# Kernel optimization log

Measured on AMD Instinct MI355X. Metric: run time of the kernel, lower is better.

The kernel has to match this reference:

```python
import jax, jax.numpy as jnp
import numpy as np

L, H, Wn, C = 2048, 768, 1024, 64


def setup_inputs() -> dict:
    key = jax.random.key(0)
    ks = jax.random.split(key, 12)
    s = 1.0 / np.sqrt(H)
    s3 = 1.0 / np.sqrt(3 * H)
    return {
        "tok_embs": jax.random.normal(ks[0], (L, H), jnp.float32),
        "wmask": jax.random.randint(ks[1], (L,), 0, Wn + 1),  # 1-indexed word positions, 0 = ignore
        "text_length": Wn,
        "label_embs": jax.random.normal(ks[2], (C, H), jnp.float32),
        "W_tok": jax.random.normal(ks[3], (H, 2 * H), jnp.float32) * s,
        "b_tok": jnp.zeros((2 * H,), jnp.float32),
        "W_lab": jax.random.normal(ks[4], (H, 2 * H), jnp.float32) * s,
        "b_lab": jnp.zeros((2 * H,), jnp.float32),
        "W1": jax.random.normal(ks[5], (3 * H, H), jnp.float32) * s3,
        "b1": jnp.zeros((H,), jnp.float32),
        "W2": jax.random.normal(ks[6], (H, 3), jnp.float32) * s,
        "b2": jnp.zeros((3,), jnp.float32),
    }


def reference(tok_embs, wmask, text_length, label_embs, W_tok, b_tok, W_lab, b_lab, W1, b1, W2, b2):
    Wd = text_length
    Hd = tok_embs.shape[-1]
    # --- word-level scatter pooling: we[wmask-1] = tok_embs where wmask > 0 ---
    # route masked-out tokens to a dummy row Wd, then drop it (jit-safe, no nonzero)
    tgt = jnp.where(wmask > 0, wmask - 1, Wd)
    we = jnp.zeros((Wd + 1, Hd), tok_embs.dtype).at[tgt].set(tok_embs)[:Wd]  # (W, H)
    # --- scorer ---
    t = (we @ W_tok + b_tok).reshape(Wd, 2, Hd)        # (W, 2, H)
    lb = (label_embs @ W_lab + b_lab).reshape(-1, 2, Hd)  # (C, 2, H)
    Cd = lb.shape[0]
    t0 = jnp.broadcast_to(t[:, None, 0, :], (Wd, Cd, Hd))
    l0 = jnp.broadcast_to(lb[None, :, 0, :], (Wd, Cd, Hd))
    prod = t[:, None, 1, :] * lb[None, :, 1, :]        # (W, C, H)
    cat = jnp.concatenate([t0, l0, prod], axis=-1)     # (W, C, 3H)
    h = jax.nn.relu(cat @ W1 + b1)                     # (W, C, H)
    scores = h @ W2 + b2                               # (W, C, 3)
    return scores
```

## Files before the change

### kernel.cpp

```cpp
#include <hip/hip_runtime.h>
#include <hip/hip_bf16.h>

static constexpr int Hd = 768;
static constexpr int H2 = 1536;
static constexpr int Cn = 64;

typedef __attribute__((ext_vector_type(8))) short short8;
typedef __attribute__((ext_vector_type(8))) _Float16 half8;
typedef __attribute__((ext_vector_type(4))) float f32x4;
typedef unsigned short us;

__device__ inline unsigned int f2bf2(float a, float b) {
    __hip_bfloat162 h = __float22bfloat162_rn(float2{a, b});
    return *reinterpret_cast<unsigned int*>(&h);
}

__device__ inline void split1(float x, us& h, us& l) {
    __hip_bfloat16 hb = __float2bfloat16(x);
    float hf = __bfloat162float(hb);
    __hip_bfloat16 lb_ = __float2bfloat16(x - hf);
    h = *reinterpret_cast<us*>(&hb);
    l = *reinterpret_cast<us*>(&lb_);
}

__device__ inline us f2b(float x) {
    __hip_bfloat16 b = __float2bfloat16(x);
    return *reinterpret_cast<us*>(&b);
}

__device__ inline us f2h(float x) {
    _Float16 h = (_Float16)x;
    return *reinterpret_cast<us*>(&h);
}

__device__ inline float b2f(us u) {
    __hip_bfloat16 b = *reinterpret_cast<__hip_bfloat16*>(&u);
    return __bfloat162float(b);
}

__device__ inline short8 hmul8(short8 a, short8 b) {
    half8 x = __builtin_bit_cast(half8, a);
    half8 y = __builtin_bit_cast(half8, b);
    half8 r = x * y;
    return __builtin_bit_cast(short8, r);
}

__device__ inline int swz(int row, int q) {
    return row * 32 + ((q ^ ((row >> 1) & 3)) << 3);
}

__device__ inline void gload16(const void* g, void* l) {
    __builtin_amdgcn_global_load_lds(
        (const __attribute__((address_space(1))) unsigned int*)g,
        (__attribute__((address_space(3))) unsigned int*)l, 16, 0, 0);
}

__global__ void k_init(int* widx, int Wd) {
    int i = blockIdx.x * 256 + threadIdx.x;
    if (i < Wd) widx[i] = -1;
}

__global__ void k_scatter(const int* __restrict__ wmask, int* widx, int L, int Wd) {
    int i = blockIdx.x * 256 + threadIdx.x;
    if (i < L) {
        int m = wmask[i];
        if (m > 0 && m <= Wd) atomicMax(&widx[m - 1], i);
    }
}

__global__ void k_build_we_split(const float4* __restrict__ tok, const int* __restrict__ widx,
                                 us* __restrict__ weh, us* __restrict__ wel, int Wd) {
    int i = blockIdx.x * 256 + threadIdx.x;
    if (i >= Wd * 192) return;
    int w = i / 192, c4 = i - w * 192;
    int idx = widx[w];
    float4 v = (idx >= 0) ? tok[idx * 192 + c4] : float4{0.f, 0.f, 0.f, 0.f};
    us hh[4], ll[4];
    split1(v.x, hh[0], ll[0]);
    split1(v.y, hh[1], ll[1]);
    split1(v.z, hh[2], ll[2]);
    split1(v.w, hh[3], ll[3]);
    size_t o = (size_t)w * Hd + c4 * 4;
    *(ushort4*)&weh[o] = ushort4{hh[0], hh[1], hh[2], hh[3]};
    *(ushort4*)&wel[o] = ushort4{ll[0], ll[1], ll[2], ll[3]};
}

struct TSArgs {
    const float* src[5];
    us* th[5];
    us* tl[5];
    int ld[5];
    int N[5];
    int fmt[5];
};
__global__ __launch_bounds__(256)
void k_tsplit(TSArgs a) {
    __shared__ float tile[64][65];
    const int z = blockIdx.z;
    const int n0 = blockIdx.x * 64, k0 = blockIdx.y * 64;
    if (n0 >= a.N[z]) return;
    const float* W = a.src[z];
    const int ld = a.ld[z];
    for (int idx = threadIdx.x; idx < 4096; idx += 256) {
        int kk = idx >> 6, nn = idx & 63;
        tile[kk][nn] = W[(size_t)(k0 + kk) * ld + n0 + nn];
    }
    __syncthreads();
    us* Th = a.th[z];
    us* Tl = a.tl[z];
    const int fmt = a.fmt[z];
    for (int idx = threadIdx.x; idx < 4096; idx += 256) {
        int nn = idx >> 6, kk = idx & 63;
        size_t o = (size_t)(n0 + nn) * Hd + k0 + kk;
        if (fmt) {
            Th[o] = f2h(tile[kk][nn]);
        } else {
            us h, l;
            split1(tile[kk][nn], h, l);
            Th[o] = h;
            Tl[o] = l;
        }
    }
}

__global__ __launch_bounds__(256)
void k_split(const float* __restrict__ x, int lda, int cols,
             us* __restrict__ h, us* __restrict__ l, int n4) {
    int i = blockIdx.x * 256 + threadIdx.x;
    if (i >= n4) return;
    int c4 = cols >> 2;
    int row = i / c4, cc = (i - row * c4) * 4;
    float4 v = *(const float4*)&x[(size_t)row * lda + cc];
    us hh[4], ll[4];
    split1(v.x, hh[0], ll[0]);
    split1(v.y, hh[1], ll[1]);
    split1(v.z, hh[2], ll[2]);
    split1(v.w, hh[3], ll[3]);
    size_t o = (size_t)row * cols + cc;
    *(ushort4*)&h[o] = ushort4{hh[0], hh[1], hh[2], hh[3]};
    *(ushort4*)&l[o] = ushort4{ll[0], ll[1], ll[2], ll[3]};
}

__global__ __launch_bounds__(256)
void k_gemm2(const us* __restrict__ Ah, const us* __restrict__ Al,
             const us* __restrict__ BhT, const us* __restrict__ BlT,
             float* __restrict__ Cpart, int M, int N, int K) {
    __shared__ __align__(16) us S[2][4][64 * 32];
    const int tid = threadIdx.x, wave = tid >> 6, lane = tid & 63;
    const int quad = lane >> 4, l15 = lane & 15;
    const int wm = wave & 1, wn = wave >> 1;
    const int m0 = blockIdx.y * 64, n0 = blockIdx.x * 64;
    const int Ks = K / gridDim.z, kbeg = blockIdx.z * Ks, kend = kbeg + Ks;
    float* C = Cpart + (size_t)blockIdx.z * M * N;

    const int srow = wave * 16 + (lane >> 2), soff = (lane & 3) * 8;
    const size_t gaB = (size_t)(m0 + srow) * K + soff;
    const size_t gbB = (size_t)(n0 + srow) * K + soff;
    const int lo = wave * 16 * 32;

    f32x4 acc[2][2];
#pragma unroll
    for (int a = 0; a < 2; ++a)
#pragma unroll
        for (int b = 0; b < 2; ++b) acc[a][b] = (f32x4){0.f, 0.f, 0.f, 0.f};

    auto stage = [&](int p, int k0) {
        gload16(Ah + gaB + k0, &S[p][0][lo]);
        gload16(Al + gaB + k0, &S[p][1][lo]);
        gload16(BhT + gbB + k0, &S[p][2][lo]);
        gload16(BlT + gbB + k0, &S[p][3][lo]);
    };

    int p = 0;
    stage(0, kbeg);
    for (int k0 = kbeg; k0 < kend; k0 += 32) {
        __syncthreads();
        if (k0 + 32 < kend) stage(p ^ 1, k0 + 32);
        short8 ah[2], al[2], bh[2], bl[2];
#pragma unroll
        for (int mt = 0; mt < 2; ++mt) {
            int off = (wm * 32 + mt * 16 + l15) * 32 + quad * 8;
            ah[mt] = *(const short8*)&S[p][0][off];
            al[mt] = *(const short8*)&S[p][1][off];
        }
#pragma unroll
        for (int nt = 0; nt < 2; ++nt) {
            int off = (wn * 32 + nt * 16 + l15) * 32 + quad * 8;
            bh[nt] = *(const short8*)&S[p][2][off];
            bl[nt] = *(const short8*)&S[p][3][off];
        }
#pragma unroll
        for (int mt = 0; mt < 2; ++mt)
#pragma unroll
            for (int nt = 0; nt < 2; ++nt) {
                acc[mt][nt] = __builtin_amdgcn_mfma_f32_16x16x32_bf16(al[mt], bh[nt], acc[mt][nt], 0, 0, 0);
                acc[mt][nt] = __builtin_amdgcn_mfma_f32_16x16x32_bf16(ah[mt], bl[nt], acc[mt][nt], 0, 0, 0);
                acc[mt][nt] = __builtin_amdgcn_mfma_f32_16x16x32_bf16(ah[mt], bh[nt], acc[mt][nt], 0, 0, 0);
            }
        p ^= 1;
    }
#pragma unroll
    for (int mt = 0; mt < 2; ++mt)
#pragma unroll
        for (int nt = 0; nt < 2; ++nt) {
            int col = n0 + wn * 32 + nt * 16 + l15;
#pragma unroll
            for (int reg = 0; reg < 4; ++reg) {
                int row = m0 + wm * 32 + mt * 16 + quad * 4 + reg;
                C[(size_t)row * N + col] = acc[mt][nt][reg];
            }
        }
}

__global__ __launch_bounds__(256)
void k_gemm3(const us* __restrict__ Ah, const us* __restrict__ Al,
             const us* __restrict__ BhT, const us* __restrict__ BlT,
             const float* __restrict__ bias, float* __restrict__ outF,
             us* __restrict__ sh, us* __restrict__ sl, us* __restrict__ bh16,
             int fp16out, int scols, int N, int K) {
    __shared__ __align__(16) us S[2][4][64 * 32];
    const int tid = threadIdx.x, wave = tid >> 6, lane = tid & 63;
    const int quad = lane >> 4, l15 = lane & 15;
    const int wm = wave & 1, wn = wave >> 1;
    const int m0 = blockIdx.y * 64, n0 = blockIdx.x * 64;

    const int srow = wave * 16 + (lane >> 2), soff = (lane & 3) * 8;
    const size_t gaB = (size_t)(m0 + srow) * K + soff;
    const size_t gbB = (size_t)(n0 + srow) * K + soff;
    const int lo = wave * 16 * 32;

    f32x4 acc[2][2];
#pragma unroll
    for (int a = 0; a < 2; ++a)
#pragma unroll
        for (int b = 0; b < 2; ++b) acc[a][b] = (f32x4){0.f, 0.f, 0.f, 0.f};

    auto stage = [&](int p, int k0) {
        gload16(Ah + gaB + k0, &S[p][0][lo]);
        gload16(Al + gaB + k0, &S[p][1][lo]);
        gload16(BhT + gbB + k0, &S[p][2][lo]);
        gload16(BlT + gbB + k0, &S[p][3][lo]);
    };

    int p = 0;
    stage(0, 0);
    for (int k0 = 0; k0 < K; k0 += 32) {
        __syncthreads();
        if (k0 + 32 < K) stage(p ^ 1, k0 + 32);
        short8 ah[2], al[2], bh[2], bl[2];
#pragma unroll
        for (int mt = 0; mt < 2; ++mt) {
            int off = (wm * 32 + mt * 16 + l15) * 32 + quad * 8;
            ah[mt] = *(const short8*)&S[p][0][off];
            al[mt] = *(const short8*)&S[p][1][off];
        }
#pragma unroll
        for (int nt = 0; nt < 2; ++nt) {
            int off = (wn * 32 + nt * 16 + l15) * 32 + quad * 8;
            bh[nt] = *(const short8*)&S[p][2][off];
            bl[nt] = *(const short8*)&S[p][3][off];
        }
#pragma unroll
        for (int mt = 0; mt < 2; ++mt)
#pragma unroll
            for (int nt = 0; nt < 2; ++nt) {
                acc[mt][nt] = __builtin_amdgcn_mfma_f32_16x16x32_bf16(al[mt], bh[nt], acc[mt][nt], 0, 0, 0);
                acc[mt][nt] = __builtin_amdgcn_mfma_f32_16x16x32_bf16(ah[mt], bl[nt], acc[mt][nt], 0, 0, 0);
                acc[mt][nt] = __builtin_amdgcn_mfma_f32_16x16x32_bf16(ah[mt], bh[nt], acc[mt][nt], 0, 0, 0);
            }
        p ^= 1;
    }
#pragma unroll
    for (int mt = 0; mt < 2; ++mt)
#pragma unroll
        for (int nt = 0; nt < 2; ++nt) {
            int col = n0 + wn * 32 + nt * 16 + l15;
            float bb = bias ? bias[col] : 0.f;
#pragma unroll
            for (int reg = 0; reg < 4; ++reg) {
                int row = m0 + wm * 32 + mt * 16 + quad * 4 + reg;
                float v = acc[mt][nt][reg] + bb;
                if (outF) outF[(size_t)row * N + col] = v;
                if (sh) {
                    if (col < scols) {
                        us h, l;
                        split1(v, h, l);
                        size_t o = (size_t)row * scols + col;
                        sh[o] = h;
                        sl[o] = l;
                    } else if (bh16) {
                        bh16[(size_t)row * scols + (col - scols)] = fp16out ? f2h(v) : f2b(v);
                    }
                }
            }
        }
}

__global__ __launch_bounds__(256)
void k_reduce(const float* __restrict__ part, int S, int MN, int N,
              const float* __restrict__ bias, float* __restrict__ outF,
              us* __restrict__ sh, us* __restrict__ sl, int scols,
              us* __restrict__ bh16, int fp16out) {
    int i = blockIdx.x * 256 + threadIdx.x;
    if (i >= MN) return;
    float v = 0.f;
    for (int s = 0; s < S; ++s) v += part[(size_t)s * MN + i];
    int row = i / N, col = i - row * N;
    if (bias) v += bias[col];
    if (outF) outF[i] = v;
    if (col < scols) {
        if (sh) {
            us h, l;
            split1(v, h, l);
            size_t o = (size_t)row * scols + col;
            sh[o] = h;
            sl[o] = l;
        }
    } else if (bh16) {
        bh16[(size_t)row * scols + (col - scols)] = fp16out ? f2h(v) : f2b(v);
    }
}

__global__ __launch_bounds__(256, 3)
void k_mfma7(const us* __restrict__ t1b,
             const us* __restrict__ W1ct,
             const us* __restrict__ lb1b,
             const float* __restrict__ Aw,
             const float* __restrict__ Bc,
             const float* __restrict__ W2,
             float* __restrict__ scr) {
    __shared__ __align__(16) us As[2][128 * 32];
    __shared__ __align__(16) us Bs[2][128 * 32];
    __shared__ float sred[128 * 3];

    const int tid = threadIdx.x, wave = tid >> 6, lane = tid & 63;
    const int quad = lane >> 4, l15 = lane & 15;
    const int wm = wave & 1, wn = wave >> 1;

    const int b = blockIdx.x;
    const int xcd = b & 7, slot = b >> 3;
    const int jx = slot >> 6;
    const int c = slot & 63;
    const int my = xcd;
    const int jt = jx * 128, m0 = my * 128;

    for (int i = tid; i < 128 * 3; i += 256) sred[i] = 0.f;

    const int aro = tid >> 1;
    const int qb = (tid & 1) * 2;
    const int kbase = qb * 8;
    const us* gA = W1ct + (size_t)(jt + aro) * Hd + kbase;
    const us* gL = lb1b + (size_t)c * Hd + kbase;
    const us* gB = t1b + (size_t)(m0 + aro) * Hd + kbase;
    const int w0 = swz(aro, qb), w1 = swz(aro, qb + 1);

    f32x4 acc[4][4];
#pragma unroll
    for (int mt = 0; mt < 4; ++mt)
#pragma unroll
        for (int nt = 0; nt < 4; ++nt) acc[mt][nt] = (f32x4){0.f, 0.f, 0.f, 0.f};

    short8 aw0l, aw0h, al0l, al0h, b0l, b0h;
    short8 aw1l, aw1h, al1l, al1h, b1l, b1h;

    aw0l = *(const short8*)(gA + 0);  aw0h = *(const short8*)(gA + 8);
    al0l = *(const short8*)(gL + 0);  al0h = *(const short8*)(gL + 8);
    b0l  = *(const short8*)(gB + 0);  b0h  = *(const short8*)(gB + 8);
    aw1l = *(const short8*)(gA + 32); aw1h = *(const short8*)(gA + 40);
    al1l = *(const short8*)(gL + 32); al1h = *(const short8*)(gL + 40);
    b1l  = *(const short8*)(gB + 32); b1h  = *(const short8*)(gB + 40);
    *(short8*)&As[0][w0] = hmul8(aw0l, al0l);
    *(short8*)&As[0][w1] = hmul8(aw0h, al0h);
    *(short8*)&Bs[0][w0] = b0l;
    *(short8*)&Bs[0][w1] = b0h;
    __syncthreads();

    for (int k = 0; k < Hd; k += 64) {
        {
            short8 af[4], bf[4];
#pragma unroll
            for (int mt = 0; mt < 4; ++mt)
                af[mt] = *(const short8*)&As[0][swz(wm * 64 + mt * 16 + l15, quad)];
#pragma unroll
            for (int nt = 0; nt < 4; ++nt)
                bf[nt] = *(const short8*)&Bs[0][swz(wn * 64 + nt * 16 + l15, quad)];
            if (k + 64 < Hd) {
                aw0l = *(const short8*)(gA + k + 64); aw0h = *(const short8*)(gA + k + 72);
                al0l = *(const short8*)(gL + k + 64); al0h = *(const short8*)(gL + k + 72);
                b0l  = *(const short8*)(gB + k + 64); b0h  = *(const short8*)(gB + k + 72);
            }
#pragma unroll
            for (int mt = 0; mt < 4; ++mt)
#pragma unroll
                for (int nt = 0; nt < 4; ++nt)
                    acc[mt][nt] = __builtin_amdgcn_mfma_f32_16x16x32_f16(
                        __builtin_bit_cast(half8, af[mt]),
                        __builtin_bit_cast(half8, bf[nt]), acc[mt][nt], 0, 0, 0);
            *(short8*)&As[1][w0] = hmul8(aw1l, al1l);
            *(short8*)&As[1][w1] = hmul8(aw1h, al1h);
            *(short8*)&Bs[1][w0] = b1l;
            *(short8*)&Bs[1][w1] = b1h;
            __syncthreads();
        }
        {
            short8 af[4], bf[4];
#pragma unroll
            for (int mt = 0; mt < 4; ++mt)
                af[mt] = *(const short8*)&As[1][swz(wm * 64 + mt * 16 + l15, quad)];
#pragma unroll
            for (int nt = 0; nt < 4; ++nt)
                bf[nt] = *(const short8*)&Bs[1][swz(wn * 64 + nt * 16 + l15, quad)];
            if (k + 96 < Hd) {
                aw1l = *(const short8*)(gA + k + 96); aw1h = *(const short8*)(gA + k + 104);
                al1l = *(const short8*)(gL + k + 96); al1h = *(const short8*)(gL + k + 104);
                b1l  = *(const short8*)(gB + k + 96); b1h  = *(const short8*)(gB + k + 104);
            }
#pragma unroll
            for (int mt = 0; mt < 4; ++mt)
#pragma unroll
                for (int nt = 0; nt < 4; ++nt)
                    acc[mt][nt] = __builtin_amdgcn_mfma_f32_16x16x32_f16(
                        __builtin_bit_cast(half8, af[mt]),
                        __builtin_bit_cast(half8, bf[nt]), acc[mt][nt], 0, 0, 0);
            if (k + 64 < Hd) {
                *(short8*)&As[0][w0] = hmul8(aw0l, al0l);
                *(short8*)&As[0][w1] = hmul8(aw0h, al0h);
                *(short8*)&Bs[0][w0] = b0l;
                *(short8*)&Bs[0][w1] = b0h;
                __syncthreads();
            }
        }
    }

    float bcv[4][4], w2v[4][4][3];
#pragma unroll
    for (int mt = 0; mt < 4; ++mt) {
        const int jb = jt + wm * 64 + mt * 16 + quad * 4;
        float4 b4 = *(const float4*)&Bc[(size_t)c * Hd + jb];
        bcv[mt][0] = b4.x; bcv[mt][1] = b4.y; bcv[mt][2] = b4.z; bcv[mt][3] = b4.w;
#pragma unroll
        for (int reg = 0; reg < 4; ++reg)
#pragma unroll
            for (int r = 0; r < 3; ++r) w2v[mt][reg][r] = W2[(jb + reg) * 3 + r];
    }
#pragma unroll
    for (int nt = 0; nt < 4; ++nt) {
        const int w = m0 + wn * 64 + nt * 16 + l15;
        const float* awp = Aw + (size_t)w * Hd + jt + wm * 64;
        float s0 = 0.f, s1 = 0.f, s2 = 0.f;
#pragma unroll
        for (int mt = 0; mt < 4; ++mt) {
            float4 a4 = *(const float4*)&awp[mt * 16 + quad * 4];
            float av[4] = {a4.x, a4.y, a4.z, a4.w};
#pragma unroll
            for (int reg = 0; reg < 4; ++reg) {
                float h = acc[mt][nt][reg] + av[reg] + bcv[mt][reg];
                h = h > 0.f ? h : 0.f;
                s0 += h * w2v[mt][reg][0];
                s1 += h * w2v[mt][reg][1];
                s2 += h * w2v[mt][reg][2];
            }
        }
        s0 += __shfl_xor(s0, 16); s0 += __shfl_xor(s0, 32);
        s1 += __shfl_xor(s1, 16); s1 += __shfl_xor(s1, 32);
        s2 += __shfl_xor(s2, 16); s2 += __shfl_xor(s2, 32);
        if (quad == 0) {
            const int wl = wn * 64 + nt * 16 + l15;
            atomicAdd(&sred[wl * 3 + 0], s0);
            atomicAdd(&sred[wl * 3 + 1], s1);
            atomicAdd(&sred[wl * 3 + 2], s2);
        }
    }
    __syncthreads();
    float* slab = scr + ((size_t)jx * 1024 * Cn + (size_t)m0 * Cn + c) * 3;
    for (int i = tid; i < 128 * 3; i += 256) {
        int wl = i / 3, r = i - wl * 3;
        slab[(size_t)wl * Cn * 3 + r] = sred[i];
    }
}

__global__ __launch_bounds__(256)
void k_scores(const float* __restrict__ scr, const float* __restrict__ b2,
              float* __restrict__ out, int n) {
    int i = blockIdx.x * 256 + threadIdx.x;
    if (i >= n) return;
    float v = b2[i % 3];
#pragma unroll
    for (int s = 0; s < 6; ++s) v += scr[(size_t)s * n + i];
    out[i] = v;
}

extern "C" void kernel_launch(void* const* d_in, const int* in_sizes, int n_in,
                              void* d_out, int out_size, void* d_ws, size_t ws_size,
                              hipStream_t stream) {
    const float* tok    = (const float*)d_in[0];
    const int*   wmask  = (const int*)d_in[1];
    const float* labe   = (const float*)d_in[3];
    const float* W_tok  = (const float*)d_in[4];
    const float* b_tok  = (const float*)d_in[5];
    const float* W_lab  = (const float*)d_in[6];
    const float* b_lab  = (const float*)d_in[7];
    const float* W1     = (const float*)d_in[8];
    const float* b1     = (const float*)d_in[9];
    const float* W2     = (const float*)d_in[10];
    const float* b2     = (const float*)d_in[11];
    float* out = (float*)d_out;

    const int L  = in_sizes[1];
    const int Wd = out_size / (Cn * 3);

    char* ws = (char*)d_ws;
    size_t off = 0;
    auto alloc = [&](size_t bytes) { char* p = ws + off; off += (bytes + 255) & ~(size_t)255; return p; };
    int*   widx  = (int*)alloc(4096);
    float* Abuf  = (float*)alloc((size_t)Wd * Hd * 4);
    float* Bbuf  = (float*)alloc((size_t)Cn * Hd * 4);
    us* W1ct  = (us*)alloc((size_t)Hd * Hd * 2);
    us* W1cl  = (us*)alloc((size_t)Hd * Hd * 2);
    us* t1b   = (us*)alloc((size_t)Wd * Hd * 2);
    us* lb1b  = (us*)alloc((size_t)Cn * Hd * 2);
    float* scr = (float*)alloc((size_t)6 * Wd * Cn * 3 * 4);
    us* WtTh  = (us*)alloc((size_t)H2 * Hd * 2);
    us* WtTl  = (us*)alloc((size_t)H2 * Hd * 2);
    us* WlTh  = (us*)alloc((size_t)H2 * Hd * 2);
    us* WlTl  = (us*)alloc((size_t)H2 * Hd * 2);
    us* W1aTh = (us*)alloc((size_t)Hd * Hd * 2);
    us* W1aTl = (us*)alloc((size_t)Hd * Hd * 2);
    us* W1bTh = (us*)alloc((size_t)Hd * Hd * 2);
    us* W1bTl = (us*)alloc((size_t)Hd * Hd * 2);
    us* weh   = (us*)alloc((size_t)Wd * Hd * 2);
    us* wel   = (us*)alloc((size_t)Wd * Hd * 2);
    us* lah   = (us*)alloc((size_t)Cn * Hd * 2);
    us* lal   = (us*)alloc((size_t)Cn * Hd * 2);
    us* t0h   = (us*)alloc((size_t)Wd * Hd * 2);
    us* t0l   = (us*)alloc((size_t)Wd * Hd * 2);
    us* lb0h  = (us*)alloc((size_t)Cn * Hd * 2);
    us* lb0l  = (us*)alloc((size_t)Cn * Hd * 2);
    float* part = (float*)alloc((size_t)8 * Cn * H2 * 4);

    k_init<<<(Wd + 255) / 256, 256, 0, stream>>>(widx, Wd);
    k_scatter<<<(L + 255) / 256, 256, 0, stream>>>(wmask, widx, L, Wd);
    k_build_we_split<<<(Wd * 192 + 255) / 256, 256, 0, stream>>>((const float4*)tok, widx, weh, wel, Wd);

    TSArgs ts;
    ts.src[0] = W_tok;  ts.th[0] = WtTh;  ts.tl[0] = WtTl;  ts.ld[0] = H2; ts.N[0] = H2; ts.fmt[0] = 0;
    ts.src[1] = W_lab;  ts.th[1] = WlTh;  ts.tl[1] = WlTl;  ts.ld[1] = H2; ts.N[1] = H2; ts.fmt[1] = 0;
    ts.src[2] = W1;                         ts.th[2] = W1aTh; ts.tl[2] = W1aTl; ts.ld[2] = Hd; ts.N[2] = Hd; ts.fmt[2] = 0;
    ts.src[3] = W1 + (size_t)Hd * Hd;       ts.th[3] = W1bTh; ts.tl[3] = W1bTl; ts.ld[3] = Hd; ts.N[3] = Hd; ts.fmt[3] = 0;
    ts.src[4] = W1 + (size_t)2 * Hd * Hd;   ts.th[4] = W1ct;  ts.tl[4] = W1cl;  ts.ld[4] = Hd; ts.N[4] = Hd; ts.fmt[4] = 1;
    k_tsplit<<<dim3(H2 / 64, Hd / 64, 5), 256, 0, stream>>>(ts);

    k_split<<<(Cn * Hd / 4 + 255) / 256, 256, 0, stream>>>(labe, Hd, Hd, lah, lal, Cn * Hd / 4);

    k_gemm3<<<dim3(H2 / 64, Wd / 64), 256, 0, stream>>>(weh, wel, WtTh, WtTl, b_tok,
                                                        nullptr, t0h, t0l, t1b, 1, Hd, H2, Hd);

    k_gemm2<<<dim3(H2 / 64, 1, 8), 256, 0, stream>>>(lah, lal, WlTh, WlTl, part, Cn, H2, Hd);
    k_reduce<<<(Cn * H2 + 255) / 256, 256, 0, stream>>>(part, 8, Cn * H2, H2, b_lab, nullptr, lb0h, lb0l, Hd, lb1b, 1);

    k_gemm3<<<dim3(Hd / 64, Wd / 64), 256, 0, stream>>>(t0h, t0l, W1aTh, W1aTl, nullptr,
                                                        Abuf, nullptr, nullptr, nullptr, 0, 0, Hd, Hd);

    k_gemm2<<<dim3(Hd / 64, 1, 8), 256, 0, stream>>>(lb0h, lb0l, W1bTh, W1bTl, part, Cn, Hd, Hd);
    k_reduce<<<(Cn * Hd + 255) / 256, 256, 0, stream>>>(part, 8, Cn * Hd, Hd, b1, Bbuf, nullptr, nullptr, Hd, nullptr, 0);

    k_mfma7<<<3072, 256, 0, stream>>>(t1b, W1ct, lb1b, Abuf, Bbuf, W2, scr);

    k_scores<<<(Wd * Cn * 3 + 255) / 256, 256, 0, stream>>>(scr, b2, out, Wd * Cn * 3);
}
```

Before: 263.9 us.

## Process two labels per block with shared tiles and direct global-to-LDS loads

The main MFMA kernel now handles two labels per block, so each staged W1c and t1 tile feeds two accumulator sets. The label-weight elementwise product moves from staging into the inner loop, applied to register fragments from a small LDS copy of both label rows. Tiles are staged with async global_load_lds over a 32-wide K double buffer, replacing the register-staged swizzled layout. The aim is to halve global and LDS staging traffic per MFMA and cut grid size, at the cost of doubled accumulator registers, lower occupancy (2 blocks per CU) and extra half-precision multiplies in the hot loop.

```diff
diff --git a/kernel.cpp b/kernel.cpp
--- a/kernel.cpp
+++ b/kernel.cpp
@@ -43,10 +43,6 @@
     half8 y = __builtin_bit_cast(half8, b);
     half8 r = x * y;
     return __builtin_bit_cast(short8, r);
-}
-
-__device__ inline int swz(int row, int q) {
-    return row * 32 + ((q ^ ((row >> 1) & 3)) << 3);
 }
 
 __device__ inline void gload16(const void* g, void* l) {
@@ -321,17 +317,18 @@
     }
 }
 
-__global__ __launch_bounds__(256, 3)
-void k_mfma7(const us* __restrict__ t1b,
+__global__ __launch_bounds__(256, 2)
+void k_mfma8(const us* __restrict__ t1b,
              const us* __restrict__ W1ct,
              const us* __restrict__ lb1b,
              const float* __restrict__ Aw,
              const float* __restrict__ Bc,
              const float* __restrict__ W2,
              float* __restrict__ scr) {
-    __shared__ __align__(16) us As[2][128 * 32];
-    __shared__ __align__(16) us Bs[2][128 * 32];
-    __shared__ float sred[128 * 3];
+    __shared__ __align__(16) us As[2][4096];
+    __shared__ __align__(16) us Bs[2][4096];
+    __shared__ __align__(16) us lbs[2][Hd];
+    __shared__ float sred[2 * 128 * 3];
 
     const int tid = threadIdx.x, wave = tid >> 6, lane = tid & 63;
     const int quad = lane >> 4, l15 = lane & 15;
@@ -339,143 +336,123 @@
 
     const int b = blockIdx.x;
     const int xcd = b & 7, slot = b >> 3;
-    const int jx = slot >> 6;
-    const int c = slot & 63;
-    const int my = xcd;
-    const int jt = jx * 128, m0 = my * 128;
-
-    for (int i = tid; i < 128 * 3; i += 256) sred[i] = 0.f;
-
-    const int aro = tid >> 1;
-    const int qb = (tid & 1) * 2;
-    const int kbase = qb * 8;
-    const us* gA = W1ct + (size_t)(jt + aro) * Hd + kbase;
-    const us* gL = lb1b + (size_t)c * Hd + kbase;
-    const us* gB = t1b + (size_t)(m0 + aro) * Hd + kbase;
-    const int w0 = swz(aro, qb), w1 = swz(aro, qb + 1);
-
-    f32x4 acc[4][4];
+    const int jx = slot >> 5;
+    const int cp = slot & 31;
+    const int c0 = cp * 2;
+    const int jt = jx * 128, m0 = xcd * 128;
+
+    for (int i = tid; i < 2 * 128 * 3; i += 256) sred[i] = 0.f;
+    if (tid < 192) {
+        int cc = tid / 96, o = (tid - cc * 96) * 8;
+        *(short8*)&lbs[cc][o] = *(const short8*)&lb1b[(size_t)(c0 + cc) * Hd + o];
+    }
+
+    const int srow = (wave & 1) * 64 + lane;
+    const int skq = (wave >> 1) * 8;
+    const us* gA = W1ct + (size_t)(jt + srow) * Hd + skq;
+    const us* gB = t1b + (size_t)(m0 + srow) * Hd + skq;
+
+    f32x4 acc0[4][4], acc1[4][4];
 #pragma unroll
     for (int mt = 0; mt < 4; ++mt)
 #pragma unroll
-        for (int nt = 0; nt < 4; ++nt) acc[mt][nt] = (f32x4){0.f, 0.f, 0.f, 0.f};
-
-    short8 aw0l, aw0h, al0l, al0h, b0l, b0h;
-    short8 aw1l, aw1h, al1l, al1h, b1l, b1h;
-
-    aw0l = *(const short8*)(gA + 0);  aw0h = *(const short8*)(gA + 8);
-    al0l = *(const short8*)(gL + 0);  al0h = *(const short8*)(gL + 8);
-    b0l  = *(const short8*)(gB + 0);  b0h  = *(const short8*)(gB + 8);
-    aw1l = *(const short8*)(gA + 32); aw1h = *(const short8*)(gA + 40);
-    al1l = *(const short8*)(gL + 32); al1h = *(const short8*)(gL + 40);
-    b1l  = *(const short8*)(gB + 32); b1h  = *(const short8*)(gB + 40);
-    *(short8*)&As[0][w0] = hmul8(aw0l, al0l);
-    *(short8*)&As[0][w1] = hmul8(aw0h, al0h);
-    *(short8*)&Bs[0][w0] = b0l;
-    *(short8*)&Bs[0][w1] = b0h;
-    __syncthreads();
-
-    for (int k = 0; k < Hd; k += 64) {
-        {
-            short8 af[4], bf[4];
-#pragma unroll
-            for (int mt = 0; mt < 4; ++mt)
-                af[mt] = *(const short8*)&As[0][swz(wm * 64 + mt * 16 + l15, quad)];
-#pragma unroll
-            for (int nt = 0; nt < 4; ++nt)
-                bf[nt] = *(const short8*)&Bs[0][swz(wn * 64 + nt * 16 + l15, quad)];
-            if (k + 64 < Hd) {
-                aw0l = *(const short8*)(gA + k + 64); aw0h = *(const short8*)(gA + k + 72);
-                al0l = *(const short8*)(gL + k + 64); al0h = *(const short8*)(gL + k + 72);
-                b0l  = *(const short8*)(gB + k + 64); b0h  = *(const short8*)(gB + k + 72);
-            }
-#pragma unroll
-            for (int mt = 0; mt < 4; ++mt)
-#pragma unroll
-                for (int nt = 0; nt < 4; ++nt)
-                    acc[mt][nt] = __builtin_amdgcn_mfma_f32_16x16x32_f16(
-                        __builtin_bit_cast(half8, af[mt]),
-                        __builtin_bit_cast(half8, bf[nt]), acc[mt][nt], 0, 0, 0);
-            *(short8*)&As[1][w0] = hmul8(aw1l, al1l);
-            *(short8*)&As[1][w1] = hmul8(aw1h, al1h);
-            *(short8*)&Bs[1][w0] = b1l;
-            *(short8*)&Bs[1][w1] = b1h;
-            __syncthreads();
-        }
-        {
-            short8 af[4], bf[4];
-#pragma unroll
-            for (int mt = 0; mt < 4; ++mt)
-                af[mt] = *(const short8*)&As[1][swz(wm * 64 + mt * 16 + l15, quad)];
-#pragma unroll
-            for (int nt = 0; nt < 4; ++nt)
-                bf[nt] = *(const short8*)&Bs[1][swz(wn * 64 + nt * 16 + l15, quad)];
-            if (k + 96 < Hd) {
-                aw1l = *(const short8*)(gA + k + 96); aw1h = *(const short8*)(gA + k + 104);
-                al1l = *(const short8*)(gL + k + 96); al1h = *(const short8*)(gL + k + 104);
-                b1l  = *(const short8*)(gB + k + 96); b1h  = *(const short8*)(gB + k + 104);
-            }
-#pragma unroll
-            for (int mt = 0; mt < 4; ++mt)
-#pragma unroll
-                for (int nt = 0; nt < 4; ++nt)
-                    acc[mt][nt] = __builtin_amdgcn_mfma_f32_16x16x32_f16(
-                        __builtin_bit_cast(half8, af[mt]),
-                        __builtin_bit_cast(half8, bf[nt]), acc[mt][nt], 0, 0, 0);
-            if (k + 64 < Hd) {
-                *(short8*)&As[0][w0] = hmul8(aw0l, al0l);
-                *(short8*)&As[0][w1] = hmul8(aw0h, al0h);
-                *(short8*)&Bs[0][w0] = b0l;
-                *(short8*)&Bs[0][w1] = b0h;
-                __syncthreads();
-            }
-        }
-    }
-
-    float bcv[4][4], w2v[4][4][3];
+        for (int nt = 0; nt < 4; ++nt) {
+            acc0[mt][nt] = (f32x4){0.f, 0.f, 0.f, 0.f};
+            acc1[mt][nt] = (f32x4){0.f, 0.f, 0.f, 0.f};
+        }
+
+    auto stage = [&](int p, int k0) {
+        gload16(gA + k0,      &As[p][wave * 512]);
+        gload16(gA + k0 + 16, &As[p][(wave + 4) * 512]);
+        gload16(gB + k0,      &Bs[p][wave * 512]);
+        gload16(gB + k0 + 16, &Bs[p][(wave + 4) * 512]);
+    };
+
+    const int rbA = quad * 1024 + (wm * 64 + l15) * 8;
+    const int rbB = quad * 1024 + (wn * 64 + l15) * 8;
+
+    stage(0, 0);
+    int p = 0;
+    for (int k0 = 0; k0 < Hd; k0 += 32) {
+        __syncthreads();
+        if (k0 + 32 < Hd) stage(p ^ 1, k0 + 32);
+        short8 af[4], bf[4];
+#pragma unroll
+        for (int mt = 0; mt < 4; ++mt) af[mt] = *(const short8*)&As[p][rbA + mt * 128];
+#pragma unroll
+        for (int nt = 0; nt < 4; ++nt) bf[nt] = *(const short8*)&Bs[p][rbB + nt * 128];
+        short8 lv0 = *(const short8*)&lbs[0][k0 + quad * 8];
+        short8 lv1 = *(const short8*)&lbs[1][k0 + quad * 8];
+#pragma unroll
+        for (int mt = 0; mt < 4; ++mt) {
+            short8 a0 = hmul8(af[mt], lv0);
+            short8 a1 = hmul8(af[mt], lv1);
+#pragma unroll
+            for (int nt = 0; nt < 4; ++nt) {
+                acc0[mt][nt] = __builtin_amdgcn_mfma_f32_16x16x32_f16(
+                    __builtin_bit_cast(half8, a0),
+                    __builtin_bit_cast(half8, bf[nt]), acc0[mt][nt], 0, 0, 0);
+                acc1[mt][nt] = __builtin_amdgcn_mfma_f32_16x16x32_f16(
+                    __builtin_bit_cast(half8, a1),
+                    __builtin_bit_cast(half8, bf[nt]), acc1[mt][nt], 0, 0, 0);
+            }
+        }
+        p ^= 1;
+    }
+
+    float bcv0[4][4], bcv1[4][4], w2v[4][4][3];
 #pragma unroll
     for (int mt = 0; mt < 4; ++mt) {
         const int jb = jt + wm * 64 + mt * 16 + quad * 4;
-        float4 b4 = *(const float4*)&Bc[(size_t)c * Hd + jb];
-        bcv[mt][0] = b4.x; bcv[mt][1] = b4.y; bcv[mt][2] = b4.z; bcv[mt][3] = b4.w;
+        float4 b4 = *(const float4*)&Bc[(size_t)c0 * Hd + jb];
+        bcv0[mt][0] = b4.x; bcv0[mt][1] = b4.y; bcv0[mt][2] = b4.z; bcv0[mt][3] = b4.w;
+        float4 b5 = *(const float4*)&Bc[(size_t)(c0 + 1) * Hd + jb];
+        bcv1[mt][0] = b5.x; bcv1[mt][1] = b5.y; bcv1[mt][2] = b5.z; bcv1[mt][3] = b5.w;
 #pragma unroll
         for (int reg = 0; reg < 4; ++reg)
 #pragma unroll
             for (int r = 0; r < 3; ++r) w2v[mt][reg][r] = W2[(jb + reg) * 3 + r];
     }
-#pragma unroll
-    for (int nt = 0; nt < 4; ++nt) {
-        const int w = m0 + wn * 64 + nt * 16 + l15;
-        const float* awp = Aw + (size_t)w * Hd + jt + wm * 64;
-        float s0 = 0.f, s1 = 0.f, s2 = 0.f;
-#pragma unroll
-        for (int mt = 0; mt < 4; ++mt) {
-            float4 a4 = *(const float4*)&awp[mt * 16 + quad * 4];
-            float av[4] = {a4.x, a4.y, a4.z, a4.w};
-#pragma unroll
-            for (int reg = 0; reg < 4; ++reg) {
-                float h = acc[mt][nt][reg] + av[reg] + bcv[mt][reg];
-                h = h > 0.f ? h : 0.f;
-                s0 += h * w2v[mt][reg][0];
-                s1 += h * w2v[mt][reg][1];
-                s2 += h * w2v[mt][reg][2];
-            }
-        }
-        s0 += __shfl_xor(s0, 16); s0 += __shfl_xor(s0, 32);
-        s1 += __shfl_xor(s1, 16); s1 += __shfl_xor(s1, 32);
-        s2 += __shfl_xor(s2, 16); s2 += __shfl_xor(s2, 32);
-        if (quad == 0) {
-            const int wl = wn * 64 + nt * 16 + l15;
-            atomicAdd(&sred[wl * 3 + 0], s0);
-            atomicAdd(&sred[wl * 3 + 1], s1);
-            atomicAdd(&sred[wl * 3 + 2], s2);
-        }
-    }
+
+    auto reduce_c = [&](const f32x4 (&ac)[4][4], const float (&bcv)[4][4], int cc) {
+#pragma unroll
+        for (int nt = 0; nt < 4; ++nt) {
+            const int w = m0 + wn * 64 + nt * 16 + l15;
+            const float* awp = Aw + (size_t)w * Hd + jt + wm * 64;
+            float s0 = 0.f, s1 = 0.f, s2 = 0.f;
+#pragma unroll
+            for (int mt = 0; mt < 4; ++mt) {
+                float4 a4 = *(const float4*)&awp[mt * 16 + quad * 4];
+                float av[4] = {a4.x, a4.y, a4.z, a4.w};
+#pragma unroll
+                for (int reg = 0; reg < 4; ++reg) {
+                    float h = ac[mt][nt][reg] + av[reg] + bcv[mt][reg];
+                    h = h > 0.f ? h : 0.f;
+                    s0 += h * w2v[mt][reg][0];
+                    s1 += h * w2v[mt][reg][1];
+                    s2 += h * w2v[mt][reg][2];
+                }
+            }
+            s0 += __shfl_xor(s0, 16); s0 += __shfl_xor(s0, 32);
+            s1 += __shfl_xor(s1, 16); s1 += __shfl_xor(s1, 32);
+            s2 += __shfl_xor(s2, 16); s2 += __shfl_xor(s2, 32);
+            if (quad == 0) {
+                const int wl = wn * 64 + nt * 16 + l15;
+                atomicAdd(&sred[cc * 384 + wl * 3 + 0], s0);
+                atomicAdd(&sred[cc * 384 + wl * 3 + 1], s1);
+                atomicAdd(&sred[cc * 384 + wl * 3 + 2], s2);
+            }
+        }
+    };
+    reduce_c(acc0, bcv0, 0);
+    reduce_c(acc1, bcv1, 1);
     __syncthreads();
-    float* slab = scr + ((size_t)jx * 1024 * Cn + (size_t)m0 * Cn + c) * 3;
-    for (int i = tid; i < 128 * 3; i += 256) {
-        int wl = i / 3, r = i - wl * 3;
-        slab[(size_t)wl * Cn * 3 + r] = sred[i];
+
+    float* slab = scr + ((size_t)jx * 1024 * Cn + (size_t)m0 * Cn) * 3;
+    for (int i = tid; i < 2 * 128 * 3; i += 256) {
+        int cc = i / 384, j = i - cc * 384;
+        int wl = j / 3, r = j - wl * 3;
+        slab[((size_t)wl * Cn + (c0 + cc)) * 3 + r] = sred[i];
     }
 }
 
@@ -564,7 +541,7 @@
     k_gemm2<<<dim3(Hd / 64, 1, 8), 256, 0, stream>>>(lb0h, lb0l, W1bTh, W1bTl, part, Cn, Hd, Hd);
     k_reduce<<<(Cn * Hd + 255) / 256, 256, 0, stream>>>(part, 8, Cn * Hd, Hd, b1, Bbuf, nullptr, nullptr, Hd, nullptr, 0);
 
-    k_mfma7<<<3072, 256, 0, stream>>>(t1b, W1ct, lb1b, Abuf, Bbuf, W2, scr);
+    k_mfma8<<<1536, 256, 0, stream>>>(t1b, W1ct, lb1b, Abuf, Bbuf, W2, scr);
 
     k_scores<<<(Wd * Cn * 3 + 255) / 256, 256, 0, stream>>>(scr, b2, out, Wd * Cn * 3);
 }
```

After: 257.8 us. 1.02x faster.
